# Optimization experiments

Measured on AMD Instinct MI355X. Metric: run time of the kernel, lower is better.

## Reference

```python
import jax, jax.numpy as jnp
import numpy as np

EPS = 1e-5  # torch InstanceNorm3d default eps


def setup_inputs() -> dict:
    key = jax.random.key(0)
    ks = jax.random.split(key, 7)
    B, C, H, W, D = 2, 128, 48, 48, 48
    c_m, c_n = 128, 64
    return {
        "x": jax.random.normal(ks[0], (B, C, H, W, D), dtype=jnp.float32),
        "WA": jax.random.normal(ks[1], (c_m, C), dtype=jnp.float32) * (1.0 / np.sqrt(C)),
        "bA": jax.random.normal(ks[2], (c_m,), dtype=jnp.float32) * 0.01,
        "WB": jax.random.normal(ks[3], (c_n, C), dtype=jnp.float32) * (1.0 / np.sqrt(C)),
        "bB": jax.random.normal(ks[4], (c_n,), dtype=jnp.float32) * 0.01,
        "WV": jax.random.normal(ks[5], (c_n, C), dtype=jnp.float32) * (1.0 / np.sqrt(C)),
        "bV": jax.random.normal(ks[6], (c_n,), dtype=jnp.float32) * 0.01,
    }


def reference(x, WA, bA, WB, bB, WV, bV):
    B, C, H, W, D = x.shape
    L = H * W * D
    xf = x.reshape(B, C, L)
    # 1x1x1 Conv3d projections == per-voxel linear over channels
    A = jnp.einsum('bcl,mc->bml', xf, WA) + bA[None, :, None]   # (B, c_m, L)
    Bm = jnp.einsum('bcl,nc->bnl', xf, WB) + bB[None, :, None]  # (B, c_n, L)
    V = jnp.einsum('bcl,nc->bnl', xf, WV) + bV[None, :, None]   # (B, c_n, L)
    # attention maps: softmax over spatial positions
    attn_maps = jax.nn.softmax(Bm, axis=-1)                     # (B, c_n, L)
    # global descriptors: A @ attn_maps^T
    G = jnp.einsum('bml,bnl->bmn', A, attn_maps)                # (B, c_m, c_n)
    # attention vectors: softmax over c_n (channel) dim
    attn_vec = jax.nn.softmax(V, axis=1)                        # (B, c_n, L)
    Z = jnp.einsum('bmn,bnl->bml', G, attn_vec)                 # (B, c_m, L)
    # InstanceNorm3d (affine=False, biased variance) per (batch, channel)
    mean = jnp.mean(Z, axis=-1, keepdims=True)
    var = jnp.var(Z, axis=-1, keepdims=True)
    Zn = (Z - mean) * jax.lax.rsqrt(var + EPS)
    return Zn.reshape(B, Z.shape[1], H, W, D)
```

## Files before the change

kernel.cpp:

```cpp
#include <hip/hip_runtime.h>

#define LTOT 110592
#define EPSV 1e-5f

typedef _Float16 f16;
typedef __attribute__((ext_vector_type(4))) _Float16 f16x4;
typedef __attribute__((ext_vector_type(8))) _Float16 f16x8;
typedef __attribute__((ext_vector_type(4))) float f32x4;

#define MFMA16(a, b, c) __builtin_amdgcn_mfma_f32_16x16x32_f16(a, b, c, 0, 0, 0)
#define SWC(c) ((((c) ^ ((c) >> 3)) & 7) << 3)

__device__ __forceinline__ f16x8 ld_w8(const float* p) {
  const float4 a = *(const float4*)p;
  const float4 b = *(const float4*)(p + 4);
  f16x8 f;
  f[0] = (f16)a.x; f[1] = (f16)a.y; f[2] = (f16)a.z; f[3] = (f16)a.w;
  f[4] = (f16)b.x; f[5] = (f16)b.y; f[6] = (f16)b.z; f[7] = (f16)b.w;
  return f;
}

__global__ __launch_bounds__(256, 2) void p1_proj_m(
    const float* __restrict__ x,
    const float* __restrict__ WB_, const float* __restrict__ bB_,
    const float* __restrict__ WV_, const float* __restrict__ bV_,
    f16* __restrict__ av_g, float* __restrict__ mpart, float* __restrict__ separt)
{
  __shared__ __align__(16) f16 XT[64 * 128 + 2240];
  __shared__ __align__(16) f16 XC[128 * 64];
  __shared__ __align__(16) f16 EL[64 * 64];
  __shared__ __align__(16) f16 AVT[64 * 64];
  __shared__ float colp[4][64];
  const int tid = threadIdx.x, b = blockIdx.y, blk = blockIdx.x;
  const int ln = tid & 63, w = tid >> 6, g = ln >> 4;

  const int nB = w * 16 + (ln & 15);
  f16x8 wbf[4], wvf[4];
  #pragma unroll
  for (int ks = 0; ks < 4; ++ks) {
    wbf[ks] = ld_w8(&WB_[nB * 128 + ks * 32 + g * 8]);
    wvf[ks] = ld_w8(&WV_[nB * 128 + ks * 32 + g * 8]);
  }
  const float sB = bB_[nB];
  float biasV[4];
  #pragma unroll
  for (int r = 0; r < 4; ++r) biasV[r] = bV_[w * 16 + g * 4 + r];

  f32x4 macc[8];
  #pragma unroll
  for (int i = 0; i < 8; ++i) macc[i] = (f32x4){0.f, 0.f, 0.f, 0.f};
  float se = 0.f;

  const int co = tid & 15, LQ = tid >> 4;
  const size_t xb = (size_t)b * 128 * LTOT;

  float4 xr[8];
  {
    const int l0 = blk * 256;
    #pragma unroll
    for (int j = 0; j < 8; ++j)
      xr[j] = *(const float4*)&x[xb + (size_t)(co * 8 + j) * LTOT + l0 + LQ * 4];
  }

  for (int t = 0; t < 4; ++t) {
    const int l0 = (blk * 4 + t) * 64;
    __syncthreads();
    #pragma unroll
    for (int i = 0; i < 4; ++i) {
      const int l = LQ * 4 + i;
      f16x8 v;
      #pragma unroll
      for (int j = 0; j < 8; ++j) v[j] = (f16)(((const float*)&xr[j])[i]);
      *(f16x8*)&XT[l * 128 + ((co * 8) ^ ((l & 7) << 3))] = v;
    }
    #pragma unroll
    for (int j = 0; j < 8; ++j) {
      const int c = co * 8 + j;
      f16x4 q;
      q[0] = (f16)xr[j].x; q[1] = (f16)xr[j].y;
      q[2] = (f16)xr[j].z; q[3] = (f16)xr[j].w;
      *(f16x4*)&XC[c * 64 + ((LQ * 4) ^ SWC(c))] = q;
    }
    __syncthreads();
    if (t < 3) {
      const int l0n = l0 + 64;
      #pragma unroll
      for (int j = 0; j < 8; ++j)
        xr[j] = *(const float4*)&x[xb + (size_t)(co * 8 + j) * LTOT + l0n + LQ * 4];
    }
    f32x4 aB[4], aV[4];
    #pragma unroll
    for (int lt = 0; lt < 4; ++lt) {
      aB[lt] = (f32x4){0.f, 0.f, 0.f, 0.f};
      aV[lt] = (f32x4){0.f, 0.f, 0.f, 0.f};
      const int l = lt * 16 + (ln & 15);
      #pragma unroll
      for (int ks = 0; ks < 4; ++ks) {
        const f16x8 xf = *(const f16x8*)&XT[l * 128 + (((ks * 4 + g) * 8) ^ ((l & 7) << 3))];
        aB[lt] = MFMA16(xf, wbf[ks], aB[lt]);
        aV[lt] = MFMA16(wvf[ks], xf, aV[lt]);
      }
    }
    #pragma unroll
    for (int lt = 0; lt < 4; ++lt) {
      f16x4 ev4;
      #pragma unroll
      for (int r = 0; r < 4; ++r) {
        const float e = __expf(aB[lt][r] + sB);
        se += e;
        ev4[r] = (f16)e;
      }
      const int lq = lt * 16 + g * 4;
      *(f16x4*)&EL[nB * 64 + (lq ^ ((nB & 7) << 3))] = ev4;
    }
    float cs[4];
    #pragma unroll
    for (int ct = 0; ct < 4; ++ct) {
      f16x4 av4;
      float s = 0.f;
      #pragma unroll
      for (int r = 0; r < 4; ++r) {
        const float e = __expf(aV[ct][r] + biasV[r]);
        s += e;
        av4[r] = (f16)e;
      }
      cs[ct] = s;
      const int l = ct * 16 + (ln & 15);
      *(f16x4*)&AVT[l * 64 + ((w * 16 + g * 4) ^ ((l & 7) << 3))] = av4;
    }
    #pragma unroll
    for (int ct = 0; ct < 4; ++ct) {
      cs[ct] += __shfl_xor(cs[ct], 16);
      cs[ct] += __shfl_xor(cs[ct], 32);
    }
    {
      const float v = (g == 0) ? cs[0] : (g == 1) ? cs[1] : (g == 2) ? cs[2] : cs[3];
      colp[w][g * 16 + (ln & 15)] = v;
    }
    __syncthreads();
    {
      const int l = tid >> 2, q = tid & 3;
      const float rs = 1.f / (colp[0][l] + colp[1][l] + colp[2][l] + colp[3][l]);
      f16x8 a0 = *(const f16x8*)&AVT[l * 64 + ((q * 16) ^ ((l & 7) << 3))];
      f16x8 a1 = *(const f16x8*)&AVT[l * 64 + ((q * 16 + 8) ^ ((l & 7) << 3))];
      #pragma unroll
      for (int j = 0; j < 8; ++j) {
        a0[j] = (f16)((float)a0[j] * rs);
        a1[j] = (f16)((float)a1[j] * rs);
      }
      f16* gp = av_g + ((size_t)b * LTOT + l0 + l) * 64 + q * 16;
      *(f16x8*)&gp[0] = a0;
      *(f16x8*)&gp[8] = a1;
    }
    {
      f16x8 el[2];
      #pragma unroll
      for (int ks = 0; ks < 2; ++ks)
        el[ks] = *(const f16x8*)&EL[nB * 64 + ((ks * 32 + g * 8) ^ ((nB & 7) << 3))];
      #pragma unroll
      for (int cblk = 0; cblk < 8; ++cblk) {
        const int c = cblk * 16 + (ln & 15);
        #pragma unroll
        for (int ks = 0; ks < 2; ++ks) {
          const f16x8 xcf = *(const f16x8*)&XC[c * 64 + ((ks * 32 + g * 8) ^ SWC(c))];
          macc[cblk] = MFMA16(el[ks], xcf, macc[cblk]);
        }
      }
    }
  }
  float* mp = mpart + (size_t)(b * 432 + blk) * 8192;
  #pragma unroll
  for (int cblk = 0; cblk < 8; ++cblk)
    #pragma unroll
    for (int r = 0; r < 4; ++r)
      mp[(w * 16 + g * 4 + r) * 128 + cblk * 16 + (ln & 15)] = macc[cblk][r];
  se += __shfl_xor(se, 16);
  se += __shfl_xor(se, 32);
  if (ln < 16) separt[(size_t)(b * 432 + blk) * 64 + w * 16 + ln] = se;
}

__global__ void p2a(const float* __restrict__ mpart, const float* __restrict__ separt,
                    float* __restrict__ mpart2, float* __restrict__ sesum)
{
  const int b = blockIdx.y, bx = blockIdx.x, tid = threadIdx.x;
  if (bx < 256) {
    const int seg = bx >> 5, chunk = bx & 31;
    const int idx = chunk * 256 + tid;
    float s = 0.f;
    for (int j = 0; j < 54; ++j)
      s += mpart[(size_t)(b * 432 + seg * 54 + j) * 8192 + idx];
    mpart2[(size_t)(b * 8 + seg) * 8192 + idx] = s;
  } else if (tid < 64) {
    float s = 0.f;
    for (int k = 0; k < 432; ++k) s += separt[(size_t)(b * 432 + k) * 64 + tid];
    sesum[b * 64 + tid] = s;
  }
}

__global__ void p2a2(const float* __restrict__ mpart2, float* __restrict__ msum)
{
  const int b = blockIdx.y;
  const int idx = blockIdx.x * 256 + threadIdx.x;
  float s = 0.f;
  #pragma unroll
  for (int k = 0; k < 8; ++k) s += mpart2[(size_t)(b * 8 + k) * 8192 + idx];
  msum[(size_t)b * 8192 + idx] = s;
}

__global__ void p2b(const float* __restrict__ WA_, const float* __restrict__ bA_,
                    const float* __restrict__ msum, const float* __restrict__ sesum,
                    float* __restrict__ g32, f16* __restrict__ g16)
{
  const int b = blockIdx.y;
  const int idx = blockIdx.x * 256 + threadIdx.x;
  const int m = idx >> 6, n = idx & 63;
  float s = 0.f;
  #pragma unroll 4
  for (int c = 0; c < 128; ++c) s += WA_[m * 128 + c] * msum[(size_t)b * 8192 + n * 128 + c];
  const float gv = s / sesum[b * 64 + n] + bA_[m];
  g32[(size_t)b * 8192 + m * 64 + n] = gv;
  g16[(size_t)b * 8192 + m * 64 + (n ^ ((m & 7) << 3))] = (f16)gv;
}

__global__ __launch_bounds__(256, 2) void p3_cov(
    const f16* __restrict__ av_g, float* __restrict__ cpart, float* __restrict__ mupart)
{
  __shared__ __align__(16) f16 AV[64 * 64];
  const int tid = threadIdx.x, b = blockIdx.y, blk = blockIdx.x;
  const int ln = tid & 63, w = tid >> 6, g = ln >> 4;
  const int nq4 = (tid & 15) * 4, lq4 = (tid >> 4) * 4;
  const int nmu = tid >> 2, qmu = tid & 3;

  f32x4 cacc[4];
  #pragma unroll
  for (int j = 0; j < 4; ++j) cacc[j] = (f32x4){0.f, 0.f, 0.f, 0.f};
  float muacc = 0.f;

  for (int t = 0; t < 8; ++t) {
    const int l0 = (blk * 8 + t) * 64;
    __syncthreads();
    {
      f16x4 rd[4];
      #pragma unroll
      for (int i = 0; i < 4; ++i)
        rd[i] = *(const f16x4*)&av_g[((size_t)b * LTOT + l0 + lq4 + i) * 64 + nq4];
      #pragma unroll
      for (int j = 0; j < 4; ++j) {
        const int n = nq4 + j;
        f16x4 wr;
        #pragma unroll
        for (int i = 0; i < 4; ++i) wr[i] = rd[i][j];
        *(f16x4*)&AV[n * 64 + (lq4 ^ ((n & 7) << 3))] = wr;
      }
    }
    __syncthreads();
    {
      const f16x8 a0 = *(const f16x8*)&AV[nmu * 64 + ((qmu * 16) ^ ((nmu & 7) << 3))];
      const f16x8 a1 = *(const f16x8*)&AV[nmu * 64 + ((qmu * 16 + 8) ^ ((nmu & 7) << 3))];
      #pragma unroll
      for (int j = 0; j < 8; ++j) muacc += (float)a0[j] + (float)a1[j];
    }
    const int nA = w * 16 + (ln & 15);
    f16x8 caf[2];
    #pragma unroll
    for (int ks = 0; ks < 2; ++ks)
      caf[ks] = *(const f16x8*)&AV[nA * 64 + ((ks * 32 + g * 8) ^ ((nA & 7) << 3))];
    #pragma unroll
    for (int nct = 0; nct < 4; ++nct) {
      const int nb = nct * 16 + (ln & 15);
      #pragma unroll
      for (int ks = 0; ks < 2; ++ks) {
        const f16x8 cbf = *(const f16x8*)&AV[nb * 64 + ((ks * 32 + g * 8) ^ ((nb & 7) << 3))];
        cacc[nct] = MFMA16(caf[ks], cbf, cacc[nct]);
      }
    }
  }
  float* cp = cpart + (size_t)(b * 216 + blk) * 4096;
  #pragma unroll
  for (int nct = 0; nct < 4; ++nct)
    #pragma unroll
    for (int r = 0; r < 4; ++r)
      cp[(w * 16 + g * 4 + r) * 64 + nct * 16 + (ln & 15)] = cacc[nct][r];
  muacc += __shfl_xor(muacc, 1);
  muacc += __shfl_xor(muacc, 2);
  if (qmu == 0) mupart[(size_t)(b * 216 + blk) * 64 + nmu] = muacc;
}

__global__ void p4a(const float* __restrict__ cpart, const float* __restrict__ mupart,
                    float* __restrict__ csum, float* __restrict__ musum)
{
  const int b = blockIdx.y, bx = blockIdx.x, tid = threadIdx.x;
  if (bx < 64) {
    const int idx = bx * 64 + (tid >> 2), q = tid & 3;
    float s = 0.f;
    for (int k = q; k < 216; k += 4) s += cpart[(size_t)(b * 216 + k) * 4096 + idx];
    s += __shfl_xor(s, 1);
    s += __shfl_xor(s, 2);
    if (q == 0) csum[(size_t)b * 4096 + idx] = s;
  } else if (tid < 64) {
    float s = 0.f;
    for (int k = 0; k < 216; ++k) s += mupart[(size_t)(b * 216 + k) * 64 + tid];
    musum[b * 64 + tid] = s;
  }
}

__global__ void p4b(const float* __restrict__ csum, const float* __restrict__ musum,
                    const float* __restrict__ g32, float* __restrict__ mr)
{
  __shared__ __align__(16) float CL[4096];
  __shared__ __align__(16) float GLs[32 * 68];
  __shared__ float MUL[64];
  const int tid = threadIdx.x, b = blockIdx.y, bx = blockIdx.x;
  #pragma unroll
  for (int k = 0; k < 16; ++k) CL[k * 256 + tid] = csum[(size_t)b * 4096 + k * 256 + tid];
  #pragma unroll
  for (int k = 0; k < 8; ++k) {
    const int idx = k * 256 + tid;
    const int m_ = idx >> 6, n_ = idx & 63;
    GLs[m_ * 68 + n_] = g32[(size_t)b * 8192 + (bx * 32 + m_) * 64 + n_];
  }
  if (tid < 64) MUL[tid] = musum[b * 64 + tid];
  __syncthreads();
  const int mrow = (tid >> 3) * 68, oct = tid & 7;
  float q = 0.f;
  #pragma unroll
  for (int q4 = 0; q4 < 2; ++q4) {
    const int npb = oct * 8 + q4 * 4;
    float t0 = 0.f, t1 = 0.f, t2 = 0.f, t3 = 0.f;
    #pragma unroll 8
    for (int n = 0; n < 64; ++n) {
      const float4 cv = *(const float4*)&CL[n * 64 + npb];
      const float gv = GLs[mrow + n];
      t0 += gv * cv.x; t1 += gv * cv.y; t2 += gv * cv.z; t3 += gv * cv.w;
    }
    const float4 gq = *(const float4*)&GLs[mrow + npb];
    q += t0 * gq.x + t1 * gq.y + t2 * gq.z + t3 * gq.w;
  }
  q += __shfl_xor(q, 1); q += __shfl_xor(q, 2); q += __shfl_xor(q, 4);
  if (oct == 0) {
    float meanq = 0.f;
    #pragma unroll 8
    for (int n = 0; n < 64; ++n) meanq += GLs[mrow + n] * MUL[n];
    const int m = bx * 32 + (tid >> 3);
    const float mean = meanq / (float)LTOT;
    const float var = fmaxf(q / (float)LTOT - mean * mean, 0.f);
    mr[(b * 128 + m) * 2] = mean;
    mr[(b * 128 + m) * 2 + 1] = rsqrtf(var + EPSV);
  }
}

__global__ __launch_bounds__(256, 2) void p5_z(
    const f16* __restrict__ av_g, const f16* __restrict__ g16,
    const float* __restrict__ mr, float* __restrict__ out)
{
  __shared__ __align__(16) f16 AVT[64 * 64];
  const int tid = threadIdx.x, b = blockIdx.y, blk = blockIdx.x;
  const int ln = tid & 63, w = tid >> 6, g = ln >> 4;
  const int lst = tid & 63, pst = tid >> 6;

  f16x8 gf[2][2];
  float mean_[2][4], rsig_[2][4];
  #pragma unroll
  for (int mct = 0; mct < 2; ++mct) {
    const int mA = w * 32 + mct * 16 + (ln & 15);
    #pragma unroll
    for (int ks = 0; ks < 2; ++ks)
      gf[mct][ks] = *(const f16x8*)&g16[(size_t)b * 8192 + mA * 64 +
                                        (((ks * 4 + g) * 8) ^ ((mA & 7) << 3))];
    #pragma unroll
    for (int r = 0; r < 4; ++r) {
      const int m = w * 32 + mct * 16 + g * 4 + r;
      mean_[mct][r] = mr[(b * 128 + m) * 2];
      rsig_[mct][r] = mr[(b * 128 + m) * 2 + 1];
    }
  }

  for (int t = 0; t < 4; ++t) {
    const int l0 = (blk * 4 + t) * 64;
    __syncthreads();
    {
      const f16* gp = av_g + ((size_t)b * LTOT + l0 + lst) * 64 + pst * 16;
      const f16x8 a0 = *(const f16x8*)&gp[0];
      const f16x8 a1 = *(const f16x8*)&gp[8];
      *(f16x8*)&AVT[lst * 64 + ((pst * 16) ^ ((lst & 7) << 3))] = a0;
      *(f16x8*)&AVT[lst * 64 + ((pst * 16 + 8) ^ ((lst & 7) << 3))] = a1;
    }
    __syncthreads();
    #pragma unroll
    for (int lt = 0; lt < 4; ++lt) {
      const int l = lt * 16 + (ln & 15);
      f16x8 avf[2];
      #pragma unroll
      for (int ks = 0; ks < 2; ++ks)
        avf[ks] = *(const f16x8*)&AVT[l * 64 + (((ks * 4 + g) * 8) ^ ((l & 7) << 3))];
      #pragma unroll
      for (int mct = 0; mct < 2; ++mct) {
        f32x4 z = {0.f, 0.f, 0.f, 0.f};
        #pragma unroll
        for (int ks = 0; ks < 2; ++ks) z = MFMA16(gf[mct][ks], avf[ks], z);
        #pragma unroll
        for (int r = 0; r < 4; ++r) {
          const int m = w * 32 + mct * 16 + g * 4 + r;
          out[(size_t)(b * 128 + m) * LTOT + l0 + l] =
              (z[r] - mean_[mct][r]) * rsig_[mct][r];
        }
      }
    }
  }
}

extern "C" void kernel_launch(void* const* d_in, const int* in_sizes, int n_in,
                              void* d_out, int out_size, void* d_ws, size_t ws_size,
                              hipStream_t stream)
{
  const float* x  = (const float*)d_in[0];
  const float* WA = (const float*)d_in[1];
  const float* bA = (const float*)d_in[2];
  const float* WB = (const float*)d_in[3];
  const float* bB = (const float*)d_in[4];
  const float* WV = (const float*)d_in[5];
  const float* bV = (const float*)d_in[6];
  float* out = (float*)d_out;

  float* w = (float*)d_ws;
  float* mpart  = w;
  float* mpart2 = mpart + 7077888;
  float* separt = mpart2 + 131072;
  float* msum   = separt + 55296;
  float* sesum  = msum + 16384;
  float* g32    = sesum + 128;
  f16*   g16f   = (f16*)(g32 + 16384);
  f16*   av_g   = g16f + 16384;
  float* cpart  = (float*)(av_g + 14155776);
  float* mupart = cpart + 1769472;
  float* csum   = mupart + 27648;
  float* musum  = csum + 8192;
  float* mr     = musum + 128;

  p1_proj_m<<<dim3(432, 2), 256, 0, stream>>>(x, WB, bB, WV, bV, av_g, mpart, separt);
  p2a<<<dim3(257, 2), 256, 0, stream>>>(mpart, separt, mpart2, sesum);
  p2a2<<<dim3(32, 2), 256, 0, stream>>>(mpart2, msum);
  p2b<<<dim3(32, 2), 256, 0, stream>>>(WA, bA, msum, sesum, g32, g16f);
  p3_cov<<<dim3(216, 2), 256, 0, stream>>>(av_g, cpart, mupart);
  p4a<<<dim3(65, 2), 256, 0, stream>>>(cpart, mupart, csum, musum);
  p4b<<<dim3(4, 2), 256, 0, stream>>>(csum, musum, g32, mr);
  p5_z<<<dim3(432, 2), 256, 0, stream>>>(av_g, g16f, mr, out);
}
```

Baseline: 128.4 us.

## Restructure V softmax in p1, fuse msum reduction into p2b, double p3 grid

In p1, the V projection is recomputed with WV staged in shared memory and each lane owning one voxel, so the channel-softmax normalisation is done with warp shuffles. This removes the AVT buffer, the colp exchange and one block barrier. The p2a2 reduction is folded into p2b, where each block re-reduces the partial M sums into shared memory; that drops a launch but repeats the reduction in all 32 blocks. p3_cov now uses 432 blocks of 4 tiles instead of 216 of 8, which adds parallelism but doubles the partial covariance buffers that p4a must reduce.

```diff
diff --git a/kernel.cpp b/kernel.cpp
--- a/kernel.cpp
+++ b/kernel.cpp
@@ -26,25 +26,33 @@
     const float* __restrict__ WV_, const float* __restrict__ bV_,
     f16* __restrict__ av_g, float* __restrict__ mpart, float* __restrict__ separt)
 {
-  __shared__ __align__(16) f16 XT[64 * 128 + 2240];
+  __shared__ __align__(16) f16 XT[64 * 128];
   __shared__ __align__(16) f16 XC[128 * 64];
   __shared__ __align__(16) f16 EL[64 * 64];
-  __shared__ __align__(16) f16 AVT[64 * 64];
-  __shared__ float colp[4][64];
+  __shared__ __align__(16) f16 WVs[64 * 128];
   const int tid = threadIdx.x, b = blockIdx.y, blk = blockIdx.x;
   const int ln = tid & 63, w = tid >> 6, g = ln >> 4;
 
   const int nB = w * 16 + (ln & 15);
-  f16x8 wbf[4], wvf[4];
-  #pragma unroll
-  for (int ks = 0; ks < 4; ++ks) {
+  f16x8 wbf[4];
+  #pragma unroll
+  for (int ks = 0; ks < 4; ++ks)
     wbf[ks] = ld_w8(&WB_[nB * 128 + ks * 32 + g * 8]);
-    wvf[ks] = ld_w8(&WV_[nB * 128 + ks * 32 + g * 8]);
-  }
   const float sB = bB_[nB];
-  float biasV[4];
-  #pragma unroll
-  for (int r = 0; r < 4; ++r) biasV[r] = bV_[w * 16 + g * 4 + r];
+  float biasV[4][4];
+  #pragma unroll
+  for (int nt = 0; nt < 4; ++nt)
+    #pragma unroll
+    for (int r = 0; r < 4; ++r) biasV[nt][r] = bV_[nt * 16 + g * 4 + r];
+
+  {
+    const int n = tid >> 2, cq = (tid & 3) * 32;
+    #pragma unroll
+    for (int j = 0; j < 4; ++j) {
+      const f16x8 v = ld_w8(&WV_[n * 128 + cq + j * 8]);
+      *(f16x8*)&WVs[n * 128 + ((cq + j * 8) ^ ((n & 7) << 3))] = v;
+    }
+  }
 
   f32x4 macc[8];
   #pragma unroll
@@ -52,6 +60,7 @@
   float se = 0.f;
 
   const int co = tid & 15, LQ = tid >> 4;
+  const int lV = w * 16 + (ln & 15);
   const size_t xb = (size_t)b * 128 * LTOT;
 
   float4 xr[8];
@@ -88,17 +97,15 @@
       for (int j = 0; j < 8; ++j)
         xr[j] = *(const float4*)&x[xb + (size_t)(co * 8 + j) * LTOT + l0n + LQ * 4];
     }
-    f32x4 aB[4], aV[4];
+    f32x4 aB[4];
     #pragma unroll
     for (int lt = 0; lt < 4; ++lt) {
       aB[lt] = (f32x4){0.f, 0.f, 0.f, 0.f};
-      aV[lt] = (f32x4){0.f, 0.f, 0.f, 0.f};
       const int l = lt * 16 + (ln & 15);
       #pragma unroll
       for (int ks = 0; ks < 4; ++ks) {
         const f16x8 xf = *(const f16x8*)&XT[l * 128 + (((ks * 4 + g) * 8) ^ ((l & 7) << 3))];
         aB[lt] = MFMA16(xf, wbf[ks], aB[lt]);
-        aV[lt] = MFMA16(wvf[ks], xf, aV[lt]);
       }
     }
     #pragma unroll
@@ -113,44 +120,41 @@
       const int lq = lt * 16 + g * 4;
       *(f16x4*)&EL[nB * 64 + (lq ^ ((nB & 7) << 3))] = ev4;
     }
-    float cs[4];
-    #pragma unroll
-    for (int ct = 0; ct < 4; ++ct) {
-      f16x4 av4;
+    f32x4 aV[4];
+    #pragma unroll
+    for (int nt = 0; nt < 4; ++nt) aV[nt] = (f32x4){0.f, 0.f, 0.f, 0.f};
+    #pragma unroll
+    for (int ks = 0; ks < 4; ++ks) {
+      const f16x8 bxf = *(const f16x8*)&XT[lV * 128 + (((ks * 4 + g) * 8) ^ ((lV & 7) << 3))];
+      #pragma unroll
+      for (int nt = 0; nt < 4; ++nt) {
+        const int nA = nt * 16 + (ln & 15);
+        const f16x8 wvf = *(const f16x8*)&WVs[nA * 128 + ((ks * 32 + g * 8) ^ ((nA & 7) << 3))];
+        aV[nt] = MFMA16(wvf, bxf, aV[nt]);
+      }
+    }
+    {
+      float ev[4][4];
       float s = 0.f;
       #pragma unroll
-      for (int r = 0; r < 4; ++r) {
-        const float e = __expf(aV[ct][r] + biasV[r]);
-        s += e;
-        av4[r] = (f16)e;
-      }
-      cs[ct] = s;
-      const int l = ct * 16 + (ln & 15);
-      *(f16x4*)&AVT[l * 64 + ((w * 16 + g * 4) ^ ((l & 7) << 3))] = av4;
-    }
-    #pragma unroll
-    for (int ct = 0; ct < 4; ++ct) {
-      cs[ct] += __shfl_xor(cs[ct], 16);
-      cs[ct] += __shfl_xor(cs[ct], 32);
-    }
-    {
-      const float v = (g == 0) ? cs[0] : (g == 1) ? cs[1] : (g == 2) ? cs[2] : cs[3];
-      colp[w][g * 16 + (ln & 15)] = v;
-    }
-    __syncthreads();
-    {
-      const int l = tid >> 2, q = tid & 3;
-      const float rs = 1.f / (colp[0][l] + colp[1][l] + colp[2][l] + colp[3][l]);
-      f16x8 a0 = *(const f16x8*)&AVT[l * 64 + ((q * 16) ^ ((l & 7) << 3))];
-      f16x8 a1 = *(const f16x8*)&AVT[l * 64 + ((q * 16 + 8) ^ ((l & 7) << 3))];
-      #pragma unroll
-      for (int j = 0; j < 8; ++j) {
-        a0[j] = (f16)((float)a0[j] * rs);
-        a1[j] = (f16)((float)a1[j] * rs);
-      }
-      f16* gp = av_g + ((size_t)b * LTOT + l0 + l) * 64 + q * 16;
-      *(f16x8*)&gp[0] = a0;
-      *(f16x8*)&gp[8] = a1;
+      for (int nt = 0; nt < 4; ++nt)
+        #pragma unroll
+        for (int r = 0; r < 4; ++r) {
+          const float e = __expf(aV[nt][r] + biasV[nt][r]);
+          ev[nt][r] = e;
+          s += e;
+        }
+      s += __shfl_xor(s, 16);
+      s += __shfl_xor(s, 32);
+      const float rs = 1.f / s;
+      f16* gp = av_g + ((size_t)b * LTOT + l0 + lV) * 64 + g * 4;
+      #pragma unroll
+      for (int nt = 0; nt < 4; ++nt) {
+        f16x4 a4;
+        #pragma unroll
+        for (int r = 0; r < 4; ++r) a4[r] = (f16)(ev[nt][r] * rs);
+        *(f16x4*)&gp[nt * 16] = a4;
+      }
     }
     {
       f16x8 el[2];
@@ -197,26 +201,25 @@
   }
 }
 
-__global__ void p2a2(const float* __restrict__ mpart2, float* __restrict__ msum)
-{
-  const int b = blockIdx.y;
-  const int idx = blockIdx.x * 256 + threadIdx.x;
-  float s = 0.f;
-  #pragma unroll
-  for (int k = 0; k < 8; ++k) s += mpart2[(size_t)(b * 8 + k) * 8192 + idx];
-  msum[(size_t)b * 8192 + idx] = s;
-}
-
-__global__ void p2b(const float* __restrict__ WA_, const float* __restrict__ bA_,
-                    const float* __restrict__ msum, const float* __restrict__ sesum,
-                    float* __restrict__ g32, f16* __restrict__ g16)
-{
-  const int b = blockIdx.y;
-  const int idx = blockIdx.x * 256 + threadIdx.x;
+__global__ void p2b2(const float* __restrict__ mpart2, const float* __restrict__ sesum,
+                     const float* __restrict__ WA_, const float* __restrict__ bA_,
+                     float* __restrict__ g32, f16* __restrict__ g16)
+{
+  __shared__ __align__(16) float MS[8192];
+  const int tid = threadIdx.x, b = blockIdx.y, bx = blockIdx.x;
+  for (int it = 0; it < 32; ++it) {
+    const int i = it * 256 + tid;
+    float s = 0.f;
+    #pragma unroll
+    for (int k = 0; k < 8; ++k) s += mpart2[(size_t)(b * 8 + k) * 8192 + i];
+    MS[i] = s;
+  }
+  __syncthreads();
+  const int idx = bx * 256 + tid;
   const int m = idx >> 6, n = idx & 63;
   float s = 0.f;
   #pragma unroll 4
-  for (int c = 0; c < 128; ++c) s += WA_[m * 128 + c] * msum[(size_t)b * 8192 + n * 128 + c];
+  for (int c = 0; c < 128; ++c) s += WA_[m * 128 + c] * MS[n * 128 + c];
   const float gv = s / sesum[b * 64 + n] + bA_[m];
   g32[(size_t)b * 8192 + m * 64 + n] = gv;
   g16[(size_t)b * 8192 + m * 64 + (n ^ ((m & 7) << 3))] = (f16)gv;
@@ -236,8 +239,8 @@
   for (int j = 0; j < 4; ++j) cacc[j] = (f32x4){0.f, 0.f, 0.f, 0.f};
   float muacc = 0.f;
 
-  for (int t = 0; t < 8; ++t) {
-    const int l0 = (blk * 8 + t) * 64;
+  for (int t = 0; t < 4; ++t) {
+    const int l0 = (blk * 4 + t) * 64;
     __syncthreads();
     {
       f16x4 rd[4];
@@ -275,7 +278,7 @@
       }
     }
   }
-  float* cp = cpart + (size_t)(b * 216 + blk) * 4096;
+  float* cp = cpart + (size_t)(b * 432 + blk) * 4096;
   #pragma unroll
   for (int nct = 0; nct < 4; ++nct)
     #pragma unroll
@@ -283,7 +286,7 @@
       cp[(w * 16 + g * 4 + r) * 64 + nct * 16 + (ln & 15)] = cacc[nct][r];
   muacc += __shfl_xor(muacc, 1);
   muacc += __shfl_xor(muacc, 2);
-  if (qmu == 0) mupart[(size_t)(b * 216 + blk) * 64 + nmu] = muacc;
+  if (qmu == 0) mupart[(size_t)(b * 432 + blk) * 64 + nmu] = muacc;
 }
 
 __global__ void p4a(const float* __restrict__ cpart, const float* __restrict__ mupart,
@@ -293,13 +296,13 @@
   if (bx < 64) {
     const int idx = bx * 64 + (tid >> 2), q = tid & 3;
     float s = 0.f;
-    for (int k = q; k < 216; k += 4) s += cpart[(size_t)(b * 216 + k) * 4096 + idx];
+    for (int k = q; k < 432; k += 4) s += cpart[(size_t)(b * 432 + k) * 4096 + idx];
     s += __shfl_xor(s, 1);
     s += __shfl_xor(s, 2);
     if (q == 0) csum[(size_t)b * 4096 + idx] = s;
   } else if (tid < 64) {
     float s = 0.f;
-    for (int k = 0; k < 216; ++k) s += mupart[(size_t)(b * 216 + k) * 64 + tid];
+    for (int k = 0; k < 432; ++k) s += mupart[(size_t)(b * 432 + k) * 64 + tid];
     musum[b * 64 + tid] = s;
   }
 }
@@ -426,22 +429,20 @@
   float* mpart  = w;
   float* mpart2 = mpart + 7077888;
   float* separt = mpart2 + 131072;
-  float* msum   = separt + 55296;
-  float* sesum  = msum + 16384;
+  float* sesum  = separt + 55296;
   float* g32    = sesum + 128;
   f16*   g16f   = (f16*)(g32 + 16384);
   f16*   av_g   = g16f + 16384;
   float* cpart  = (float*)(av_g + 14155776);
-  float* mupart = cpart + 1769472;
-  float* csum   = mupart + 27648;
+  float* mupart = cpart + 3538944;
+  float* csum   = mupart + 55296;
   float* musum  = csum + 8192;
   float* mr     = musum + 128;
 
   p1_proj_m<<<dim3(432, 2), 256, 0, stream>>>(x, WB, bB, WV, bV, av_g, mpart, separt);
   p2a<<<dim3(257, 2), 256, 0, stream>>>(mpart, separt, mpart2, sesum);
-  p2a2<<<dim3(32, 2), 256, 0, stream>>>(mpart2, msum);
-  p2b<<<dim3(32, 2), 256, 0, stream>>>(WA, bA, msum, sesum, g32, g16f);
-  p3_cov<<<dim3(216, 2), 256, 0, stream>>>(av_g, cpart, mupart);
+  p2b2<<<dim3(32, 2), 256, 0, stream>>>(mpart2, sesum, WA, bA, g32, g16f);
+  p3_cov<<<dim3(432, 2), 256, 0, stream>>>(av_g, cpart, mupart);
   p4a<<<dim3(65, 2), 256, 0, stream>>>(cpart, mupart, csum, musum);
   p4b<<<dim3(4, 2), 256, 0, stream>>>(csum, musum, g32, mr);
   p5_z<<<dim3(432, 2), 256, 0, stream>>>(av_g, g16f, mr, out);
```

After: 169.0 us. 31.7% more time.
